# Performance work log

Hardware: AMD Instinct MI355X
Metric: run time of the kernel (lower is better)

The kernel has to match this reference:

```python
import jax, jax.numpy as jnp
import numpy as np

K = 8  # kernel_size
COUT = 512


def setup_inputs() -> dict:
    key = jax.random.key(0)
    k1, k2, k3 = jax.random.split(key, 3)
    B, CIN, L = 8, 512, 2048
    x = jax.random.normal(k1, (B, CIN, L), dtype=jnp.float32)
    # nn.Linear(CIN, COUT*K) weight, scaled like kaiming-uniform-ish init
    W = jax.random.normal(k2, (COUT * K, CIN), dtype=jnp.float32) * (1.0 / np.sqrt(CIN))
    b = jax.random.normal(k3, (COUT,), dtype=jnp.float32)
    return {"x": x, "W": W, "b": b}


def reference(x, W, b):
    # x: (B, Cin, L); W: (Cout*K, Cin) with row layout j = k*Cout + co; b: (Cout,)
    B, Cin, L = x.shape
    # pointwise linear expand: (B, Cout*K, L)
    z = jnp.einsum('bcl,oc->bol', x, W)
    z = z.reshape(B, K, COUT, L)  # k-major channel layout
    # causal overlap-add fold: y[b,co,t] = sum_k z[b,k,co,t-k]
    y = z[:, 0]
    for k in range(1, K):  # small fixed kernel-size loop
        y = y.at[:, :, k:].add(z[:, k, :, : L - k])
    return y + b[None, :, None]
```

## Files before the change

### kernel.cpp

```cpp
#include <hip/hip_runtime.h>
#include <hip/hip_bf16.h>
#include <cstdint>
#include <cstddef>

#define CIN   512
#define COUT  512
#define LLEN  2048
#define BATCH 8
#define KTAP  8
#define LPAD  (LLEN + 8)

typedef __bf16 bf16x8_t __attribute__((ext_vector_type(8)));
typedef float  f32x4_t  __attribute__((ext_vector_type(4)));
typedef unsigned short u16x8_t __attribute__((ext_vector_type(8)));

__device__ __forceinline__ unsigned short f2bf(float f) {
  __bf16 h = (__bf16)f;
  return __builtin_bit_cast(unsigned short, h);
}

__device__ __forceinline__ void gl2lds16(unsigned short* lds, const unsigned short* g) {
  __builtin_amdgcn_global_load_lds(
      (const __attribute__((address_space(1))) unsigned int*)g,
      (__attribute__((address_space(3))) unsigned int*)lds,
      16, 0, 0);
}

__global__ __launch_bounds__(256) void prepass_kernel(
    const float* __restrict__ x, unsigned short* __restrict__ xtp,
    const float4* __restrict__ W, u16x8_t* __restrict__ Wb) {
  const int bid = blockIdx.x;
  const int t   = threadIdx.x;

  if (bid >= 2048) {
    int idx = (bid - 2048) * 256 + t;
    float4 a = W[idx * 2], b = W[idx * 2 + 1];
    u16x8_t o;
    o[0] = f2bf(a.x); o[1] = f2bf(a.y); o[2] = f2bf(a.z); o[3] = f2bf(a.w);
    o[4] = f2bf(b.x); o[5] = f2bf(b.y); o[6] = f2bf(b.z); o[7] = f2bf(b.w);
    Wb[idx] = o;
    return;
  }

  __shared__ float tile[64][65];
  const int b  = bid >> 8;
  const int c0 = ((bid >> 5) & 7) * 64;
  const int l0 = (bid & 31) * 64;

  if ((bid & 31) == 0 && t < 64) {
    unsigned short* hp = xtp + ((size_t)b * LPAD + (t >> 3)) * CIN + c0 + (t & 7) * 8;
    *(u16x8_t*)hp = (u16x8_t){0, 0, 0, 0, 0, 0, 0, 0};
  }

  {
    const int cr = t >> 2;
    const int lv = (t & 3) * 16;
    const float* src = x + ((size_t)b * CIN + c0 + cr) * LLEN + l0 + lv;
#pragma unroll
    for (int i = 0; i < 4; ++i) {
      float4 v = *(const float4*)(src + 4 * i);
      tile[cr][lv + 4 * i + 0] = v.x;
      tile[cr][lv + 4 * i + 1] = v.y;
      tile[cr][lv + 4 * i + 2] = v.z;
      tile[cr][lv + 4 * i + 3] = v.w;
    }
  }
  __syncthreads();
  {
    const int l    = t >> 2;
    const int cseg = (t & 3) * 16;
    unsigned short ov[16];
#pragma unroll
    for (int u = 0; u < 16; ++u) ov[u] = f2bf(tile[cseg + u][l]);
    unsigned short* dst = xtp + ((size_t)b * LPAD + 8 + l0 + l) * CIN + c0 + cseg;
    *(u16x8_t*)dst       = *(const u16x8_t*)&ov[0];
    *(u16x8_t*)(dst + 8) = *(const u16x8_t*)&ov[8];
  }
}


__global__ __launch_bounds__(256) void conv_gemm_kernel(
    const unsigned short* __restrict__ Wb,
    const unsigned short* __restrict__ xtp,
    const float* __restrict__ bias,
    float* __restrict__ y)
{
  __shared__ __align__(16) unsigned short As[2][128 * 64];
  __shared__ __align__(16) unsigned short Bs[2][136 * 64];

  const int t    = threadIdx.x;
  const int lane = t & 63;
  const int wid  = t >> 6;
  const int wm   = wid & 1, wn = wid >> 1;
  const int l0   = blockIdx.x * 128;
  const int o0   = blockIdx.y * 128;
  const int b    = blockIdx.z;

  const int quad = lane >> 4;
  const int lrow = lane & 15;

  f32x4_t acc[4][4];
#pragma unroll
  for (int i = 0; i < 4; ++i)
#pragma unroll
    for (int j = 0; j < 4; ++j)
      acc[i][j] = (f32x4_t){0.f, 0.f, 0.f, 0.f};

  const int srow    = t >> 3;
  const int schunk  = (t & 7) ^ (srow & 7);
  const int lds_off = t * 8;

  const unsigned short* xb = xtp + (size_t)b * LPAD * CIN;

  auto stage_A = [&](int kk, int buf) {
    const unsigned short* asrc =
        Wb + (size_t)((kk & 7) * COUT + o0 + srow) * CIN + (kk >> 3) * 64 + schunk * 8;
#pragma unroll
    for (int rd = 0; rd < 4; ++rd)
      gl2lds16(&As[buf][0] + lds_off + rd * 2048, asrc + (size_t)rd * 32 * CIN);
  };
  auto stage_B = [&](int ct, int buf) {
    const int c0 = ct * 64;
    const unsigned short* src = xb + (size_t)(l0 + srow) * CIN + c0 + schunk * 8;
#pragma unroll
    for (int rd = 0; rd < 4; ++rd)
      gl2lds16(&Bs[buf][0] + lds_off + rd * 2048, src + (size_t)rd * 32 * CIN);
    if (t < 64) {
      const int r2  = 128 + (t >> 3);
      const int ch2 = (t & 7) ^ (r2 & 7);
      gl2lds16(&Bs[buf][0] + 128 * 64 + t * 8,
               xb + (size_t)(l0 + r2) * CIN + c0 + ch2 * 8);
    }
  };

  stage_B(0, 0);
  stage_A(0, 0);
  __syncthreads();

#pragma unroll 1
  for (int kk = 0; kk < 64; ++kk) {
    const int k  = kk & 7;
    const int ct = kk >> 3;
    if (kk + 1 < 64) stage_A(kk + 1, (kk + 1) & 1);
    if (k == 7 && ct + 1 < 8) stage_B(ct + 1, (ct + 1) & 1);

    const unsigned short* Ac = &As[kk & 1][0];
    const unsigned short* Bc = &Bs[ct & 1][0];
#pragma unroll
    for (int h = 0; h < 2; ++h) {
      bf16x8_t af[4], bfr[4];
#pragma unroll
      for (int i = 0; i < 4; ++i) {
        int row  = wm * 64 + i * 16 + lrow;
        int slot = (h * 4 + quad) ^ (row & 7);
        af[i] = *(const bf16x8_t*)(Ac + row * 64 + slot * 8);
      }
#pragma unroll
      for (int j = 0; j < 4; ++j) {
        int row  = (8 - k) + wn * 64 + j * 16 + lrow;
        int slot = (h * 4 + quad) ^ (row & 7);
        bfr[j] = *(const bf16x8_t*)(Bc + row * 64 + slot * 8);
      }
#pragma unroll
      for (int i = 0; i < 4; ++i)
#pragma unroll
        for (int j = 0; j < 4; ++j)
          acc[i][j] = __builtin_amdgcn_mfma_f32_16x16x32_bf16(af[i], bfr[j], acc[i][j], 0, 0, 0);
    }
    __syncthreads();
  }

#pragma unroll
  for (int i = 0; i < 4; ++i) {
    const int o_base = o0 + wm * 64 + i * 16 + quad * 4;
    const float4 bv = *(const float4*)(bias + o_base);
    const float bvr[4] = {bv.x, bv.y, bv.z, bv.w};
#pragma unroll
    for (int j = 0; j < 4; ++j) {
      const int l = l0 + wn * 64 + j * 16 + lrow;
#pragma unroll
      for (int r = 0; r < 4; ++r) {
        y[((size_t)b * COUT + o_base + r) * LLEN + l] = acc[i][j][r] + bvr[r];
      }
    }
  }
}


extern "C" void kernel_launch(void* const* d_in, const int* in_sizes, int n_in,
                              void* d_out, int out_size, void* d_ws, size_t ws_size,
                              hipStream_t stream) {
  const float* x    = (const float*)d_in[0];
  const float* W    = (const float*)d_in[1];
  const float* bias = (const float*)d_in[2];
  float* y          = (float*)d_out;

  unsigned short* xtp = (unsigned short*)d_ws;
  unsigned short* Wb  = (unsigned short*)((char*)d_ws +
                        (size_t)BATCH * LPAD * CIN * sizeof(unsigned short));

  prepass_kernel<<<2048 + 1024, 256, 0, stream>>>(
      x, xtp, (const float4*)W, (u16x8_t*)Wb);
  conv_gemm_kernel<<<dim3(LLEN / 128, COUT / 128, BATCH), 256, 0, stream>>>(
      Wb, xtp, bias, y);
}
```

Before: 149.9 us.

## Switch GEMM to 32x32x16 MFMA with two waves per block

Replaces the 16x16x32 bf16 MFMA tiling with 32x32x16 MFMA instructions and cuts the block from four waves to two. Each wave now computes a 128x64 output slab, and the LDS staging loops are widened to eight loads per thread. The larger MFMA shape is meant to reduce LDS fragment reads per FLOP and raise MFMA efficiency. In exchange each wave holds more accumulators (128 floats), which raises register pressure, and fewer waves per block means less latency hiding.

```diff
diff --git a/kernel.cpp b/kernel.cpp
--- a/kernel.cpp
+++ b/kernel.cpp
@@ -11,7 +11,7 @@
 #define LPAD  (LLEN + 8)
 
 typedef __bf16 bf16x8_t __attribute__((ext_vector_type(8)));
-typedef float  f32x4_t  __attribute__((ext_vector_type(4)));
+typedef float  f32x16_t __attribute__((ext_vector_type(16)));
 typedef unsigned short u16x8_t __attribute__((ext_vector_type(8)));
 
 __device__ __forceinline__ unsigned short f2bf(float f) {
@@ -79,7 +79,7 @@
 }
 
 
-__global__ __launch_bounds__(256) void conv_gemm_kernel(
+__global__ __launch_bounds__(128) void conv_gemm_kernel(
     const unsigned short* __restrict__ Wb,
     const unsigned short* __restrict__ xtp,
     const float* __restrict__ bias,
@@ -90,21 +90,20 @@
 
   const int t    = threadIdx.x;
   const int lane = t & 63;
-  const int wid  = t >> 6;
-  const int wm   = wid & 1, wn = wid >> 1;
+  const int wv   = t >> 6;
   const int l0   = blockIdx.x * 128;
   const int o0   = blockIdx.y * 128;
   const int b    = blockIdx.z;
 
-  const int quad = lane >> 4;
-  const int lrow = lane & 15;
-
-  f32x4_t acc[4][4];
+  const int ln31 = lane & 31;
+  const int hi   = lane >> 5;
+
+  f32x16_t acc[4][2];
 #pragma unroll
   for (int i = 0; i < 4; ++i)
 #pragma unroll
-    for (int j = 0; j < 4; ++j)
-      acc[i][j] = (f32x4_t){0.f, 0.f, 0.f, 0.f};
+    for (int j = 0; j < 2; ++j)
+      acc[i][j] = (f32x16_t)(0.f);
 
   const int srow    = t >> 3;
   const int schunk  = (t & 7) ^ (srow & 7);
@@ -116,15 +115,15 @@
     const unsigned short* asrc =
         Wb + (size_t)((kk & 7) * COUT + o0 + srow) * CIN + (kk >> 3) * 64 + schunk * 8;
 #pragma unroll
-    for (int rd = 0; rd < 4; ++rd)
-      gl2lds16(&As[buf][0] + lds_off + rd * 2048, asrc + (size_t)rd * 32 * CIN);
+    for (int rd = 0; rd < 8; ++rd)
+      gl2lds16(&As[buf][0] + lds_off + rd * 1024, asrc + (size_t)rd * 16 * CIN);
   };
   auto stage_B = [&](int ct, int buf) {
     const int c0 = ct * 64;
     const unsigned short* src = xb + (size_t)(l0 + srow) * CIN + c0 + schunk * 8;
 #pragma unroll
-    for (int rd = 0; rd < 4; ++rd)
-      gl2lds16(&Bs[buf][0] + lds_off + rd * 2048, src + (size_t)rd * 32 * CIN);
+    for (int rd = 0; rd < 8; ++rd)
+      gl2lds16(&Bs[buf][0] + lds_off + rd * 1024, src + (size_t)rd * 16 * CIN);
     if (t < 64) {
       const int r2  = 128 + (t >> 3);
       const int ch2 = (t & 7) ^ (r2 & 7);
@@ -146,41 +145,46 @@
 
     const unsigned short* Ac = &As[kk & 1][0];
     const unsigned short* Bc = &Bs[ct & 1][0];
-#pragma unroll
-    for (int h = 0; h < 2; ++h) {
-      bf16x8_t af[4], bfr[4];
-#pragma unroll
-      for (int i = 0; i < 4; ++i) {
-        int row  = wm * 64 + i * 16 + lrow;
-        int slot = (h * 4 + quad) ^ (row & 7);
-        af[i] = *(const bf16x8_t*)(Ac + row * 64 + slot * 8);
+    const int bshift = 8 - k;
+
+#pragma unroll
+    for (int s = 0; s < 4; ++s) {
+      bf16x8_t af[4], bf[2];
+#pragma unroll
+      for (int mi = 0; mi < 4; ++mi) {
+        int row  = mi * 32 + ln31;
+        int slot = (s * 2 + hi) ^ (row & 7);
+        af[mi] = *(const bf16x8_t*)(Ac + row * 64 + slot * 8);
       }
 #pragma unroll
-      for (int j = 0; j < 4; ++j) {
-        int row  = (8 - k) + wn * 64 + j * 16 + lrow;
-        int slot = (h * 4 + quad) ^ (row & 7);
-        bfr[j] = *(const bf16x8_t*)(Bc + row * 64 + slot * 8);
+      for (int nj = 0; nj < 2; ++nj) {
+        int row  = bshift + wv * 64 + nj * 32 + ln31;
+        int slot = (s * 2 + hi) ^ (row & 7);
+        bf[nj] = *(const bf16x8_t*)(Bc + row * 64 + slot * 8);
       }
 #pragma unroll
-      for (int i = 0; i < 4; ++i)
-#pragma unroll
-        for (int j = 0; j < 4; ++j)
-          acc[i][j] = __builtin_amdgcn_mfma_f32_16x16x32_bf16(af[i], bfr[j], acc[i][j], 0, 0, 0);
+      for (int mi = 0; mi < 4; ++mi)
+#pragma unroll
+        for (int nj = 0; nj < 2; ++nj)
+          acc[mi][nj] = __builtin_amdgcn_mfma_f32_32x32x16_bf16(af[mi], bf[nj], acc[mi][nj], 0, 0, 0);
     }
     __syncthreads();
   }
 
 #pragma unroll
-  for (int i = 0; i < 4; ++i) {
-    const int o_base = o0 + wm * 64 + i * 16 + quad * 4;
-    const float4 bv = *(const float4*)(bias + o_base);
-    const float bvr[4] = {bv.x, bv.y, bv.z, bv.w};
-#pragma unroll
-    for (int j = 0; j < 4; ++j) {
-      const int l = l0 + wn * 64 + j * 16 + lrow;
-#pragma unroll
-      for (int r = 0; r < 4; ++r) {
-        y[((size_t)b * COUT + o_base + r) * LLEN + l] = acc[i][j][r] + bvr[r];
+  for (int mi = 0; mi < 4; ++mi) {
+#pragma unroll
+    for (int rq = 0; rq < 4; ++rq) {
+      const int o_base = o0 + mi * 32 + rq * 8 + 4 * hi;
+      const float4 bv = *(const float4*)(bias + o_base);
+      const float bvr[4] = {bv.x, bv.y, bv.z, bv.w};
+#pragma unroll
+      for (int nj = 0; nj < 2; ++nj) {
+        const int l = l0 + wv * 64 + nj * 32 + ln31;
+#pragma unroll
+        for (int r0 = 0; r0 < 4; ++r0) {
+          y[((size_t)b * COUT + o_base + r0) * LLEN + l] = acc[mi][nj][rq * 4 + r0] + bvr[r0];
+        }
       }
     }
   }
@@ -201,6 +205,6 @@
 
   prepass_kernel<<<2048 + 1024, 256, 0, stream>>>(
       x, xtp, (const float4*)W, (u16x8_t*)Wb);
-  conv_gemm_kernel<<<dim3(LLEN / 128, COUT / 128, BATCH), 256, 0, stream>>>(
+  conv_gemm_kernel<<<dim3(LLEN / 128, COUT / 128, BATCH), 128, 0, stream>>>(
       Wb, xtp, bias, y);
 }
```

Result: slower. 167.3 us (+11.6%).
